# Kernel tuning notes

Hardware: AMD Instinct MI355X
Metric: run time of the kernel (lower is better)

The kernel has to match this reference:

```python
import jax, jax.numpy as jnp
import numpy as np

H, W = 64, 64

def _fft_mask(h, w):
    # matches torch: W -> W//2+1 for rfft; linspace(-1,1,H) x linspace(0,1,W//2+1)
    wr = w // 2 + 1
    ys = np.linspace(-1.0, 1.0, h)
    xs = np.linspace(0.0, 1.0, wr)
    Y, X = np.meshgrid(ys, xs, indexing='ij')
    return (np.abs(X) < 0.1) | (np.abs(Y) < 0.1) | (X ** 2 + Y ** 2 <= 0.4 ** 2)

_MASK = _fft_mask(H, W)
_IY, _IX = np.nonzero(_MASK)            # static gather indices, K = mask.sum()
_K = int(_MASK.sum())


def setup_inputs() -> dict:
    key = jax.random.key(0)
    k1, k2, k3 = jax.random.split(key, 3)
    S, P, C = 16, 256, 3
    enc_dim = 1024
    mask_dim = 6 * _K                    # real+imag, C=3 channels -> 2*3*K
    x = jax.random.normal(k1, (S, P, C, H, W), dtype=jnp.float32)
    bc_mask = jnp.zeros((H, W), dtype=bool)
    proj_w = jax.random.normal(k2, (enc_dim, mask_dim), dtype=jnp.float32) / np.sqrt(mask_dim)
    proj_b = jax.random.normal(k3, (enc_dim,), dtype=jnp.float32) * 0.01
    return {"x": x, "bc_mask": bc_mask, "proj_w": proj_w, "proj_b": proj_b}


def reference(x, bc_mask, proj_w, proj_b):
    S, P, C = x.shape[0], x.shape[1], x.shape[2]
    fft_x = jnp.fft.rfft2(x)                       # (S,P,C,H,W//2+1) complex
    fft_x = jnp.fft.fftshift(fft_x, axes=-2)       # shift along H
    # boolean-mask gather (row-major over (H, W//2+1) per (s,p,c)), then flatten C*K
    filt = fft_x[..., _IY, _IX]                    # (S,P,C,K)
    filt = filt.reshape(S, P, C * _K)
    feats = jnp.concatenate([jnp.real(filt), jnp.imag(filt)], axis=-1)  # (S,P,6K)
    return feats @ proj_w.T + proj_b               # (S,P,enc_dim)
```

## Files before the change

kernel.cpp:

```cpp
#include <hip/hip_runtime.h>
#include <hip/hip_bf16.h>
#include <math.h>

typedef float f32x4 __attribute__((ext_vector_type(4)));
typedef __bf16 bf16x8 __attribute__((ext_vector_type(8)));

#define PI2 6.283185307179586

static __device__ __forceinline__ unsigned short f2b(float f) {
  __hip_bfloat16 h = __float2bfloat16(f);
  return reinterpret_cast<unsigned short&>(h);
}

__global__ __launch_bounds__(256) void setup_tables_kernel(
    int* __restrict__ post, __hip_bfloat16* __restrict__ Tt,
    __hip_bfloat16* __restrict__ Ub) {
  const int tid = threadIdx.x;
  __shared__ int cnt[64];
  __shared__ int pref[64];

  if (tid < 64) {
    int i = tid;
    double ys = -1.0 + (double)i * (2.0 / 63.0);
    int cRow = 0;
    for (int j = 0; j < 33; ++j) {
      double xs = (double)j / 32.0;
      bool m = (fabs(xs) < 0.1) || (fabs(ys) < 0.1) || (xs * xs + ys * ys <= 0.16);
      cRow += m ? 1 : 0;
    }
    cnt[i] = cRow;
  }
  __syncthreads();
  if (tid == 0) {
    int s = 0;
    for (int i = 0; i < 64; ++i) { pref[i] = s; s += cnt[i]; }
  }
  __syncthreads();
  if (tid < 64) {
    int i = tid;
    int k = pref[i];
    double ys = -1.0 + (double)i * (2.0 / 63.0);
    for (int j = 0; j < 36; ++j) {
      int v = -1;
      if (j < 33) {
        double xs = (double)j / 32.0;
        bool m = (fabs(xs) < 0.1) || (fabs(ys) < 0.1) || (xs * xs + ys * ys <= 0.16);
        if (m) v = k++;
      }
      post[i * 36 + j] = v;
    }
  }

  for (int idx = tid; idx < 80 * 64; idx += 256) {
    int n = idx >> 6, w = idx & 63;
    float v = 0.0f;
    if (n < 33) {
      int r = (n * w) & 63;
      v = cosf((float)(PI2 / 64.0) * (float)r);
    } else if (n >= 40 && n < 73) {
      int r = ((n - 40) * w) & 63;
      v = -sinf((float)(PI2 / 64.0) * (float)r);
    }
    Tt[idx] = __float2bfloat16(v);
  }

  for (int idx = tid; idx < 128 * 128; idx += 256) {
    int up = idx >> 7, kk = idx & 127;
    int u = up & 63;
    int vfreq = (u + 32) & 63;
    int h = kk & 63;
    int r = (vfreq * h) & 63;
    float cv, sv;
    __sincosf((float)(PI2 / 64.0) * (float)r, &sv, &cv);
    float val;
    if (up < 64) val = (kk < 64) ? cv : sv;
    else         val = (kk < 64) ? -sv : cv;
    Ub[idx] = __float2bfloat16(val);
  }
}

__global__ __launch_bounds__(256) void wconv_kernel(
    const float* __restrict__ W, __hip_bfloat16* __restrict__ wB,
    int N, int Kd, int Kp) {
  int total = N * Kp;
  for (int idx = blockIdx.x * 256 + threadIdx.x; idx < total; idx += gridDim.x * 256) {
    int e = idx / Kp;
    int f = idx - e * Kp;
    float v = (f < Kd) ? W[(size_t)e * Kd + f] : 0.0f;
    wB[idx] = __float2bfloat16(v);
  }
}

#define WAVES 4
#define WBUF 8704

__global__ __launch_bounds__(256) void fft_mfma_kernel(
    const float* __restrict__ x,
    const __hip_bfloat16* __restrict__ Tt,
    const __hip_bfloat16* __restrict__ Ub,
    const int* __restrict__ post,
    __hip_bfloat16* __restrict__ feats,
    int K, int Kp) {
  __shared__ __align__(16) char lds[WAVES * WBUF];
  const int tid = threadIdx.x;
  const int lane = tid & 63;
  const int w = tid >> 6;
  const int l4 = lane & 15;
  const int q = lane >> 4;
  const int img = blockIdx.x * WAVES + w;
  const int sp = img / 3;
  const int c = img - sp * 3;
  char* buf = lds + w * WBUF;

  {
    const float* xi = x + (size_t)img * 4096;
    #pragma unroll
    for (int i = 0; i < 16; ++i) {
      float4 v = *reinterpret_cast<const float4*>(xi + i * 256 + lane * 4);
      int h = i * 4 + q;
      int k = l4 * 4;
      int off = h * 128 + (((k >> 3) ^ (h & 7)) * 16 + (k & 7) * 2);
      ushort4 b;
      b.x = f2b(v.x); b.y = f2b(v.y); b.z = f2b(v.z); b.w = f2b(v.w);
      *reinterpret_cast<ushort4*>(buf + off) = b;
    }
  }

  f32x4 acc1[4][5] = {};
  #pragma unroll
  for (int ks = 0; ks < 2; ++ks) {
    bf16x8 a1[4], b1[5];
    #pragma unroll
    for (int m = 0; m < 4; ++m) {
      int h = m * 16 + l4;
      int kg = ks * 4 + q;
      a1[m] = *reinterpret_cast<const bf16x8*>(buf + h * 128 + ((kg ^ (h & 7)) * 16));
    }
    #pragma unroll
    for (int n = 0; n < 5; ++n) {
      int row = n * 16 + l4;
      b1[n] = *reinterpret_cast<const bf16x8*>(
          (const char*)Tt + row * 128 + ks * 64 + q * 16);
    }
    #pragma unroll
    for (int m = 0; m < 4; ++m)
      #pragma unroll
      for (int n = 0; n < 5; ++n)
        acc1[m][n] = __builtin_amdgcn_mfma_f32_16x16x32_bf16(a1[m], b1[n], acc1[m][n], 0, 0, 0);
  }

  #pragma unroll
  for (int n = 0; n < 5; ++n) {
    int col = n * 16 + l4;
    bool isRe = (col < 33);
    bool isIm = (col >= 40 && col < 73);
    if (!(isRe || isIm)) continue;
    int j = isRe ? col : (col - 40);
    #pragma unroll
    for (int m = 0; m < 4; ++m) {
      #pragma unroll
      for (int r = 0; r < 4; ++r) {
        int h = m * 16 + q * 4 + r;
        int kk = isRe ? h : (h + 64);
        int off = j * 256 + (((kk >> 3) ^ (j & 15)) * 16 + (kk & 7) * 2);
        *reinterpret_cast<unsigned short*>(buf + off) = f2b(acc1[m][n][r]);
      }
    }
  }

  f32x4 acc2[3][8] = {};
  #pragma unroll
  for (int ks = 0; ks < 4; ++ks) {
    bf16x8 a2[3], b2[8];
    #pragma unroll
    for (int m = 0; m < 3; ++m) {
      int j = m * 16 + l4;
      if (j > 33) j = 33;
      int kg = ks * 4 + q;
      a2[m] = *reinterpret_cast<const bf16x8*>(buf + j * 256 + ((kg ^ (j & 15)) * 16));
    }
    #pragma unroll
    for (int n = 0; n < 8; ++n) {
      int row = n * 16 + l4;
      b2[n] = *reinterpret_cast<const bf16x8*>(
          (const char*)Ub + row * 256 + ks * 64 + q * 16);
    }
    #pragma unroll
    for (int m = 0; m < 3; ++m)
      #pragma unroll
      for (int n = 0; n < 8; ++n)
        acc2[m][n] = __builtin_amdgcn_mfma_f32_16x16x32_bf16(a2[m], b2[n], acc2[m][n], 0, 0, 0);
  }

  #pragma unroll
  for (int n = 0; n < 8; ++n) {
    int up = n * 16 + l4;
    int u = up & 63;
    int base = (up >> 6) ? K : 0;
    #pragma unroll
    for (int m = 0; m < 3; ++m) {
      int j0 = m * 16 + q * 4;
      if (j0 >= 33) continue;
      int4 kv = *reinterpret_cast<const int4*>(post + u * 36 + j0);
      #pragma unroll
      for (int r = 0; r < 4; ++r) {
        int j = j0 + r;
        int k = (&kv.x)[r];
        if (j < 33 && k >= 0)
          *reinterpret_cast<unsigned short*>(buf + (base + k) * 2) = f2b(acc2[m][n][r]);
      }
    }
  }

  {
    size_t obase = (size_t)sp * Kp;
    const unsigned int* fb = reinterpret_cast<const unsigned int*>(buf);
    unsigned int* gRe = reinterpret_cast<unsigned int*>(feats + obase + (size_t)c * K);
    unsigned int* gIm = reinterpret_cast<unsigned int*>(feats + obase + (size_t)3 * K + (size_t)c * K);
    const int KD2 = K / 2;
    for (int i = lane; i < KD2; i += 64) {
      gRe[i] = fb[i];
      gIm[i] = fb[KD2 + i];
    }
    if (c == 2) {
      unsigned int* gp = reinterpret_cast<unsigned int*>(feats + obase + (size_t)6 * K);
      int padDw = (Kp - 6 * K) / 2;
      for (int i = lane; i < padDw; i += 64) gp[i] = 0u;
    }
  }
}

#define BM 128
#define BN 128
#define BKK 64

__global__ __launch_bounds__(256) void gemm_bias_kernel(
    const __hip_bfloat16* __restrict__ A, const __hip_bfloat16* __restrict__ B,
    const float* __restrict__ bias, float* __restrict__ C,
    int M, int N, int Kp) {
  __shared__ __align__(16) unsigned short As[BM * BKK];
  __shared__ __align__(16) unsigned short Bs[BN * BKK];

  const int tid = threadIdx.x;
  const int lane = tid & 63;
  const int wid = tid >> 6;
  const int wm = wid & 1;
  const int wn = wid >> 1;
  const int nbm = M / BM;
  const int bm = blockIdx.x % nbm;
  const int bn = blockIdx.x / nbm;
  const int row0A = bm * BM;
  const int row0B = bn * BN;

  f32x4 acc[4][4] = {};

  for (int k0 = 0; k0 < Kp; k0 += BKK) {
    #pragma unroll
    for (int i = 0; i < 4; ++i) {
      int qc = i * 256 + tid;
      int r = qc >> 3;
      int cb = (qc & 7) * 16;
      const char* gA = (const char*)A + ((size_t)(row0A + r) * Kp + k0) * 2 + cb;
      const char* gB = (const char*)B + ((size_t)(row0B + r) * Kp + k0) * 2 + cb;
      char* lA = (char*)As + (size_t)(i * 256 + wid * 64) * 16;
      char* lB = (char*)Bs + (size_t)(i * 256 + wid * 64) * 16;
      __builtin_amdgcn_global_load_lds((const __attribute__((address_space(1))) void*)gA,
                                       (__attribute__((address_space(3))) void*)lA, 16, 0, 0);
      __builtin_amdgcn_global_load_lds((const __attribute__((address_space(1))) void*)gB,
                                       (__attribute__((address_space(3))) void*)lB, 16, 0, 0);
    }
    __syncthreads();

    #pragma unroll
    for (int kk = 0; kk < 2; ++kk) {
      bf16x8 afr[4], bfr[4];
      const int ke = kk * 32 + (lane >> 4) * 8;
      #pragma unroll
      for (int m = 0; m < 4; ++m) {
        int rowA = wm * 64 + m * 16 + (lane & 15);
        afr[m] = *reinterpret_cast<const bf16x8*>(&As[rowA * BKK + ke]);
      }
      #pragma unroll
      for (int n = 0; n < 4; ++n) {
        int rowB = wn * 64 + n * 16 + (lane & 15);
        bfr[n] = *reinterpret_cast<const bf16x8*>(&Bs[rowB * BKK + ke]);
      }
      #pragma unroll
      for (int m = 0; m < 4; ++m)
        #pragma unroll
        for (int n = 0; n < 4; ++n)
          acc[m][n] = __builtin_amdgcn_mfma_f32_16x16x32_bf16(afr[m], bfr[n], acc[m][n], 0, 0, 0);
    }
    __syncthreads();
  }

  #pragma unroll
  for (int n = 0; n < 4; ++n) {
    int gcol = row0B + wn * 64 + n * 16 + (lane & 15);
    float bv = bias[gcol];
    #pragma unroll
    for (int m = 0; m < 4; ++m) {
      int grow0 = row0A + wm * 64 + m * 16 + (lane >> 4) * 4;
      #pragma unroll
      for (int r = 0; r < 4; ++r) {
        C[(size_t)(grow0 + r) * N + gcol] = acc[m][n][r] + bv;
      }
    }
  }
}

extern "C" void kernel_launch(void* const* d_in, const int* in_sizes, int n_in,
                              void* d_out, int out_size, void* d_ws, size_t ws_size,
                              hipStream_t stream) {
  const float* x = (const float*)d_in[0];
  const float* W = (const float*)d_in[2];
  const float* bias = (const float*)d_in[3];
  float* out = (float*)d_out;

  const int ENC = in_sizes[3];
  const int Kd = in_sizes[2] / ENC;
  const int K = Kd / 6;
  const int NIMG = in_sizes[0] / 4096;
  const int SP = NIMG / 3;
  const int Kp = (Kd + 63) & ~63;

  char* ws = (char*)d_ws;
  int* post = (int*)ws;
  __hip_bfloat16* Tt = (__hip_bfloat16*)(ws + 9216);
  __hip_bfloat16* Ub = (__hip_bfloat16*)(ws + 19456);
  __hip_bfloat16* wB = (__hip_bfloat16*)(ws + 52224);
  size_t wBytes = (size_t)ENC * Kp * 2;
  __hip_bfloat16* feats = (__hip_bfloat16*)(ws + 52224 + wBytes);

  setup_tables_kernel<<<1, 256, 0, stream>>>(post, Tt, Ub);
  wconv_kernel<<<1024, 256, 0, stream>>>(W, wB, ENC, Kd, Kp);
  fft_mfma_kernel<<<NIMG / WAVES, 256, 0, stream>>>(x, Tt, Ub, post, feats, K, Kp);
  gemm_bias_kernel<<<(SP / BM) * (ENC / BN), 256, 0, stream>>>(feats, wB, bias, out, SP, ENC, Kp);
}
```

Baseline: 214.9 us.

## Stage FFT input via global_load_lds and cache compact mask index table in LDS

```diff
diff --git a/kernel.cpp b/kernel.cpp
--- a/kernel.cpp
+++ b/kernel.cpp
@@ -13,7 +13,7 @@
 }
 
 __global__ __launch_bounds__(256) void setup_tables_kernel(
-    int* __restrict__ post, __hip_bfloat16* __restrict__ Tt,
+    unsigned short* __restrict__ post16, __hip_bfloat16* __restrict__ Tt,
     __hip_bfloat16* __restrict__ Ub) {
   const int tid = threadIdx.x;
   __shared__ int cnt[64];
@@ -41,13 +41,13 @@
     int k = pref[i];
     double ys = -1.0 + (double)i * (2.0 / 63.0);
     for (int j = 0; j < 36; ++j) {
-      int v = -1;
+      unsigned short v = 0xFFFFu;
       if (j < 33) {
         double xs = (double)j / 32.0;
         bool m = (fabs(xs) < 0.1) || (fabs(ys) < 0.1) || (xs * xs + ys * ys <= 0.16);
-        if (m) v = k++;
-      }
-      post[i * 36 + j] = v;
+        if (m) v = (unsigned short)(k++);
+      }
+      post16[i * 36 + j] = v;
     }
   }
 
@@ -91,17 +91,18 @@
   }
 }
 
-#define WAVES 4
-#define WBUF 8704
-
-__global__ __launch_bounds__(256) void fft_mfma_kernel(
+#define WAVES 2
+#define WBUF 16384
+#define POSTB 4608
+
+__global__ __launch_bounds__(128) void fft_mfma_kernel(
     const float* __restrict__ x,
     const __hip_bfloat16* __restrict__ Tt,
     const __hip_bfloat16* __restrict__ Ub,
-    const int* __restrict__ post,
+    const unsigned short* __restrict__ post16,
     __hip_bfloat16* __restrict__ feats,
     int K, int Kp) {
-  __shared__ __align__(16) char lds[WAVES * WBUF];
+  __shared__ __align__(16) char lds[WAVES * WBUF + POSTB];
   const int tid = threadIdx.x;
   const int lane = tid & 63;
   const int w = tid >> 6;
@@ -111,19 +112,34 @@
   const int sp = img / 3;
   const int c = img - sp * 3;
   char* buf = lds + w * WBUF;
+  unsigned short* postl = reinterpret_cast<unsigned short*>(lds + WAVES * WBUF);
 
   {
     const float* xi = x + (size_t)img * 4096;
     #pragma unroll
-    for (int i = 0; i < 16; ++i) {
-      float4 v = *reinterpret_cast<const float4*>(xi + i * 256 + lane * 4);
-      int h = i * 4 + q;
-      int k = l4 * 4;
-      int off = h * 128 + (((k >> 3) ^ (h & 7)) * 16 + (k & 7) * 2);
-      ushort4 b;
-      b.x = f2b(v.x); b.y = f2b(v.y); b.z = f2b(v.z); b.w = f2b(v.w);
-      *reinterpret_cast<ushort4*>(buf + off) = b;
-    }
+    for (int r = 0; r < 16; ++r) {
+      const float* g = xi + r * 256 + lane * 4;
+      __builtin_amdgcn_global_load_lds(
+          (const __attribute__((address_space(1))) void*)g,
+          (__attribute__((address_space(3))) void*)(buf + r * 1024), 16, 0, 0);
+    }
+  }
+  {
+    const unsigned int* src = reinterpret_cast<const unsigned int*>(post16);
+    unsigned int* dst = reinterpret_cast<unsigned int*>(postl);
+    for (int i = tid; i < (64 * 36) / 2; i += 128) dst[i] = src[i];
+  }
+  asm volatile("s_waitcnt vmcnt(0)" ::: "memory");
+  __syncthreads();
+
+  #pragma unroll
+  for (int r = 0; r < 16; ++r) {
+    float4 v = *reinterpret_cast<const float4*>(buf + r * 1024 + lane * 16);
+    int h = r * 4 + (lane >> 4);
+    int woff = h * 128 + (((l4 >> 1) ^ (h & 7)) * 16 + (l4 & 1) * 8);
+    ushort4 b;
+    b.x = f2b(v.x); b.y = f2b(v.y); b.z = f2b(v.z); b.w = f2b(v.w);
+    *reinterpret_cast<ushort4*>(buf + woff) = b;
   }
 
   f32x4 acc1[4][5] = {};
@@ -201,13 +217,13 @@
     for (int m = 0; m < 3; ++m) {
       int j0 = m * 16 + q * 4;
       if (j0 >= 33) continue;
-      int4 kv = *reinterpret_cast<const int4*>(post + u * 36 + j0);
+      ushort4 kv = *reinterpret_cast<const ushort4*>(postl + u * 36 + j0);
       #pragma unroll
       for (int r = 0; r < 4; ++r) {
         int j = j0 + r;
-        int k = (&kv.x)[r];
+        short k = (short)((&kv.x)[r]);
         if (j < 33 && k >= 0)
-          *reinterpret_cast<unsigned short*>(buf + (base + k) * 2) = f2b(acc2[m][n][r]);
+          *reinterpret_cast<unsigned short*>(buf + ((int)k + base) * 2) = f2b(acc2[m][n][r]);
       }
     }
   }
@@ -325,15 +341,15 @@
   const int Kp = (Kd + 63) & ~63;
 
   char* ws = (char*)d_ws;
-  int* post = (int*)ws;
+  unsigned short* post16 = (unsigned short*)ws;
   __hip_bfloat16* Tt = (__hip_bfloat16*)(ws + 9216);
   __hip_bfloat16* Ub = (__hip_bfloat16*)(ws + 19456);
   __hip_bfloat16* wB = (__hip_bfloat16*)(ws + 52224);
   size_t wBytes = (size_t)ENC * Kp * 2;
   __hip_bfloat16* feats = (__hip_bfloat16*)(ws + 52224 + wBytes);
 
-  setup_tables_kernel<<<1, 256, 0, stream>>>(post, Tt, Ub);
+  setup_tables_kernel<<<1, 256, 0, stream>>>(post16, Tt, Ub);
   wconv_kernel<<<1024, 256, 0, stream>>>(W, wB, ENC, Kd, Kp);
-  fft_mfma_kernel<<<NIMG / WAVES, 256, 0, stream>>>(x, Tt, Ub, post, feats, K, Kp);
+  fft_mfma_kernel<<<NIMG / WAVES, 128, 0, stream>>>(x, Tt, Ub, post16, feats, K, Kp);
   gemm_bias_kernel<<<(SP / BM) * (ENC / BN), 256, 0, stream>>>(feats, wB, bias, out, SP, ENC, Kp);
 }
```

Measured after the change: 189.0 us. -12.0%, faster.
